# Kernel tuning notes

Measured on AMD Instinct MI355X. Metric: run time of the kernel, lower is better.

## Reference

```python
import jax, jax.numpy as jnp
import numpy as np

NUM_V, NUM_R, ARITY = 100000, 1000, 3
D, I, H = 128, 64, 128
B, N = 4096, 64


def setup_inputs() -> dict:
    key = jax.random.key(0)
    ks = jax.random.split(key, 11)
    return {
        "r": jax.random.randint(ks[0], (B, N), 0, NUM_R),
        "e": jax.random.randint(ks[1], (ARITY, B, N), 0, NUM_V),
        "V": jax.random.normal(ks[2], (NUM_V, D + I), dtype=jnp.float32),
        "R": jax.random.normal(ks[3], (NUM_R, D), dtype=jnp.float32),
        "P": jax.random.normal(ks[4], (ARITY, D), dtype=jnp.float32),
        "WV": jax.random.normal(ks[5], (D + I, H), dtype=jnp.float32) * (1.0 / np.sqrt(D + I)),
        "bV": jax.random.normal(ks[6], (H,), dtype=jnp.float32) * 0.01,
        "WR": jax.random.normal(ks[7], (D, H), dtype=jnp.float32) * (1.0 / np.sqrt(D)),
        "bR": jax.random.normal(ks[8], (H,), dtype=jnp.float32) * 0.01,
        "WP": jax.random.normal(ks[9], (D, H), dtype=jnp.float32) * (1.0 / np.sqrt(D)),
        "bP": jax.random.normal(ks[10], (H,), dtype=jnp.float32) * 0.01,
    }


def reference(r, e, V, R, P, WV, bV, WR, bR, WP, bP):
    # x = Rl(R[r]) : gather relation embeddings then project -> [B, N, H]
    x = jnp.einsum("bnd,dh->bnh", R[r], WR) + bR
    # Pl(P[i]) for all arity positions at once -> [A, H]
    pe = P @ WP + bP
    # Vl(V[e[i]]) for all positions: gather then project -> [A, B, N, H]
    ve = jnp.einsum("abnd,dh->abnh", V[e], WV) + bV
    # loop body x = x * Pl(P[i]) * Vl(V[e[i]]) == product over arity axis
    x = x * jnp.prod(pe[:, None, None, :] * ve, axis=0)
    # dropout is identity (p=0 / eval); reduce over neighbor axis
    return jnp.sum(x, axis=1)  # [B, H]
```

## Files before the change

### kernel.cpp

```cpp
#include <hip/hip_runtime.h>

#define NUM_V 100000
#define NUM_R 1000
#define ARITY 3
#define DD 128
#define DI 192
#define HH 128
#define BB 4096
#define NN 64

typedef __attribute__((ext_vector_type(4))) float f32x4;
typedef __attribute__((ext_vector_type(8))) _Float16 half8;
typedef __attribute__((ext_vector_type(2))) _Float16 half2v;

__device__ inline void gload16(const void* g, void* lds) {
    __builtin_amdgcn_global_load_lds(
        (const __attribute__((address_space(1))) unsigned int*)g,
        (__attribute__((address_space(3))) unsigned int*)lds, 16, 0, 0);
}

__global__ __launch_bounds__(256) void prep_kernel(
    const float* __restrict__ R, const float* __restrict__ WR, const float* __restrict__ bR,
    _Float16* __restrict__ RWh,
    const float* __restrict__ WV, unsigned short* __restrict__ wf,
    const float* __restrict__ P, const float* __restrict__ WP, const float* __restrict__ bP,
    float* __restrict__ peProd) {
    const int bid = blockIdx.x;
    const int tid = threadIdx.x;

    if (bid < 32) {
        const int lane = tid & 63;
        const int wave = tid >> 6;
        const int wavesPerGrid = 32 * 4;
        const int waveId = bid * 4 + wave;
        const float2 b2 = ((const float2*)bR)[lane];
        const float2* __restrict__ W2 = (const float2*)WR;
        for (int rowBase0 = waveId * 8; rowBase0 < NUM_R; rowBase0 += wavesPerGrid * 8) {
            const int rowBase = __builtin_amdgcn_readfirstlane(rowBase0);
            float2 acc[8];
#pragma unroll
            for (int r8 = 0; r8 < 8; ++r8) acc[r8] = make_float2(0.f, 0.f);
#pragma unroll 4
            for (int k4 = 0; k4 < DD / 4; ++k4) {
                float4 v[8];
#pragma unroll
                for (int r8 = 0; r8 < 8; ++r8)
                    v[r8] = ((const float4*)(R + (size_t)(rowBase + r8) * DD))[k4];
#pragma unroll
                for (int kk = 0; kk < 4; ++kk) {
                    float2 w = W2[(k4 * 4 + kk) * 64 + lane];
#pragma unroll
                    for (int r8 = 0; r8 < 8; ++r8) {
                        float vv = (kk == 0) ? v[r8].x : (kk == 1) ? v[r8].y : (kk == 2) ? v[r8].z : v[r8].w;
                        acc[r8].x += vv * w.x;
                        acc[r8].y += vv * w.y;
                    }
                }
            }
#pragma unroll
            for (int r8 = 0; r8 < 8; ++r8) {
                if (rowBase + r8 < NUM_R) {
                    half2v h;
                    h.x = (_Float16)(acc[r8].x + b2.x);
                    h.y = (_Float16)(acc[r8].y + b2.y);
                    *(half2v*)(RWh + (size_t)(rowBase + r8) * HH + lane * 2) = h;
                }
            }
        }
    } else if (bid < 80) {
        if (tid < 64) {
            const int wb = bid - 32;
            const int ks = wb >> 3;
            const int ct = wb & 7;
            const int l = tid;
            const int col = ct * 16 + (l & 15);
            const int k0 = ks * 32 + (l >> 4) * 8;
            size_t base = (size_t)(ks * 8 + ct) * 512;
#pragma unroll
            for (int j = 0; j < 8; ++j) {
                float v = WV[(size_t)(k0 + j) * HH + col];
                wf[base + l * 8 + j] = __builtin_bit_cast(unsigned short, (_Float16)v);
            }
        }
    } else {
        if (tid < HH) {
            int h = tid;
            float prod = 1.0f;
            for (int a = 0; a < ARITY; ++a) {
                float acc = bP[h];
                for (int d = 0; d < DD; ++d) acc += P[a * DD + d] * WP[d * HH + h];
                prod *= acc;
            }
            peProd[h] = prod;
        }
    }
}

__global__ __launch_bounds__(832, 6) void gemm_bres(const float* __restrict__ A,
                                                    const unsigned short* __restrict__ wf,
                                                    const float* __restrict__ bias,
                                                    _Float16* __restrict__ C, int M) {
    __shared__ unsigned short bsm[24576];

    const int tid = threadIdx.x;
    const int l = tid & 63;
    const int wv = tid >> 6;

    const int tile = wv * 512 + blockIdx.x;
    const int rowbase = tile * 16;
    const bool active = rowbase < M;

    float bcol[8];
#pragma unroll
    for (int ct = 0; ct < 8; ++ct) bcol[ct] = bias[ct * 16 + (l & 15)];

    const float* aptr;
    {
        int rr = rowbase + (l & 15);
        if (rr >= M) rr = M - 1;
        aptr = A + (size_t)rr * DI + (l >> 4) * 8;
    }

    f32x4 acc[8];
#pragma unroll
    for (int ct = 0; ct < 8; ++ct) acc[ct] = (f32x4){0.f, 0.f, 0.f, 0.f};

    float4 va[3][2];
#define LOAD_A(buf, ks)                                   \
    do {                                                  \
        va[buf][0] = *(const float4*)(aptr + (ks) * 32);  \
        va[buf][1] = *(const float4*)(aptr + (ks) * 32 + 4); \
    } while (0)

    if (active) {
        LOAD_A(0, 0);
        LOAD_A(1, 1);
    }

    if (wv < 12) {
#pragma unroll
        for (int i = 0; i < 4; ++i) {
            const int off = wv * 4096 + i * 1024;
            gload16((const char*)wf + off + l * 16, (char*)bsm + off);
        }
    }

    __syncthreads();
    if (!active) return;

#pragma unroll
    for (int ks = 0; ks < 6; ++ks) {
        const int cur = ks % 3;
        if (ks < 4) LOAD_A((ks + 2) % 3, ks + 2);

        half8 ah;
        {
            half8 t;
            t[0] = (_Float16)va[cur][0].x;
            t[1] = (_Float16)va[cur][0].y;
            t[2] = (_Float16)va[cur][0].z;
            t[3] = (_Float16)va[cur][0].w;
            t[4] = (_Float16)va[cur][1].x;
            t[5] = (_Float16)va[cur][1].y;
            t[6] = (_Float16)va[cur][1].z;
            t[7] = (_Float16)va[cur][1].w;
            ah = t;
        }

#pragma unroll
        for (int ct = 0; ct < 8; ++ct) {
            const int fb = (ks * 8 + ct) * 512;
            half8 bh = *(const half8*)&bsm[fb + l * 8];
            acc[ct] = __builtin_amdgcn_mfma_f32_16x16x32_f16(ah, bh, acc[ct], 0, 0, 0);
        }
    }
#undef LOAD_A

    {
        const int rb = rowbase + (l >> 4) * 4;
#pragma unroll
        for (int j = 0; j < 4; ++j) {
            const int row = rb + j;
            if (row < M) {
#pragma unroll
                for (int ct = 0; ct < 8; ++ct)
                    C[(size_t)row * HH + ct * 16 + (l & 15)] = (_Float16)(acc[ct][j] + bcol[ct]);
            }
        }
    }
}

__global__ __launch_bounds__(256) void gather_kernel(const int* __restrict__ r,
                                                     const int* __restrict__ e,
                                                     const _Float16* __restrict__ VWh,
                                                     const _Float16* __restrict__ RWh,
                                                     const float* __restrict__ peProd,
                                                     float* __restrict__ out) {
    __shared__ int rIdx[NN];
    __shared__ int eIdx[ARITY][NN];
    __shared__ float4 partial[3][16][2];

    const int b = blockIdx.x;
    const int tid = threadIdx.x;

    if (tid < NN) {
        rIdx[tid] = r[b * NN + tid];
    } else {
        int t = tid - NN;
        eIdx[t >> 6][t & 63] = e[(size_t)(t >> 6) * BB * NN + b * NN + (t & 63)];
    }
    __syncthreads();

    const int lane = tid & 63;
    const int wv = tid >> 6;
    const int q = lane >> 4;
    const int ho = lane & 15;

    float acc8[8];
#pragma unroll
    for (int k = 0; k < 8; ++k) acc8[k] = 0.f;

#pragma unroll
    for (int it = 0; it < 4; ++it) {
        int n = it * 16 + wv * 4 + q;
        half8 rw = *(const half8*)(RWh + (size_t)rIdx[n] * HH + ho * 8);
        half8 v0 = *(const half8*)(VWh + (size_t)eIdx[0][n] * HH + ho * 8);
        half8 v1 = *(const half8*)(VWh + (size_t)eIdx[1][n] * HH + ho * 8);
        half8 v2 = *(const half8*)(VWh + (size_t)eIdx[2][n] * HH + ho * 8);
        half8 p = rw * v0;
        p = p * v1;
        p = p * v2;
#pragma unroll
        for (int k = 0; k < 8; ++k) acc8[k] += (float)p[k];
    }

#pragma unroll
    for (int k = 0; k < 8; ++k) {
        acc8[k] += __shfl_xor(acc8[k], 16);
        acc8[k] += __shfl_xor(acc8[k], 32);
    }

    if (wv > 0 && lane < 16) {
        partial[wv - 1][ho][0] = make_float4(acc8[0], acc8[1], acc8[2], acc8[3]);
        partial[wv - 1][ho][1] = make_float4(acc8[4], acc8[5], acc8[6], acc8[7]);
    }
    __syncthreads();
    if (wv == 0 && lane < 16) {
        float4 s0 = make_float4(acc8[0], acc8[1], acc8[2], acc8[3]);
        float4 s1 = make_float4(acc8[4], acc8[5], acc8[6], acc8[7]);
#pragma unroll
        for (int g = 0; g < 3; ++g) {
            float4 t0 = partial[g][ho][0], t1 = partial[g][ho][1];
            s0.x += t0.x; s0.y += t0.y; s0.z += t0.z; s0.w += t0.w;
            s1.x += t1.x; s1.y += t1.y; s1.z += t1.z; s1.w += t1.w;
        }
        float4 p0 = ((const float4*)peProd)[ho * 2];
        float4 p1 = ((const float4*)peProd)[ho * 2 + 1];
        ((float4*)(out + (size_t)b * HH))[ho * 2] =
            make_float4(s0.x * p0.x, s0.y * p0.y, s0.z * p0.z, s0.w * p0.w);
        ((float4*)(out + (size_t)b * HH))[ho * 2 + 1] =
            make_float4(s1.x * p1.x, s1.y * p1.y, s1.z * p1.z, s1.w * p1.w);
    }
}

extern "C" void kernel_launch(void* const* d_in, const int* in_sizes, int n_in,
                              void* d_out, int out_size, void* d_ws, size_t ws_size,
                              hipStream_t stream) {
    const int* r = (const int*)d_in[0];
    const int* e = (const int*)d_in[1];
    const float* V = (const float*)d_in[2];
    const float* R = (const float*)d_in[3];
    const float* P = (const float*)d_in[4];
    const float* WV = (const float*)d_in[5];
    const float* bV = (const float*)d_in[6];
    const float* WR = (const float*)d_in[7];
    const float* bR = (const float*)d_in[8];
    const float* WP = (const float*)d_in[9];
    const float* bP = (const float*)d_in[10];
    float* out = (float*)d_out;

    _Float16* VWh = (_Float16*)d_ws;
    _Float16* RWh = VWh + (size_t)NUM_V * HH;
    float* peProd = (float*)(RWh + (size_t)NUM_R * HH);
    unsigned short* wfrag = (unsigned short*)(peProd + HH);

    prep_kernel<<<81, 256, 0, stream>>>(R, WR, bR, RWh, WV, wfrag, P, WP, bP, peProd);
    gemm_bres<<<512, 832, 0, stream>>>(V, wfrag, bV, VWh, NUM_V);
    gather_kernel<<<BB, 256, 0, stream>>>(r, e, VWh, RWh, peProd, out);
}
```

Measured before the change: 68.71 us.

## Fuse prep kernel into V-projection GEMM and convert WV fragments in-block

Removes the separate prep kernel launch. Each GEMM block now converts WV from fp32 into the fp16 fragment layout directly in LDS, replacing the async global-to-LDS copy of a precomputed fragment buffer. The R projection and the arity product are appended to the tail of the GEMM blocks, spread across 500 blocks plus one extra block. This saves a launch and a dependency, but every block now redoes the strided WV conversion, and the tail blocks run a serial scalar dot-product loop that may lengthen the critical path.

```diff
diff --git a/kernel.cpp b/kernel.cpp
--- a/kernel.cpp
+++ b/kernel.cpp
@@ -13,106 +13,26 @@
 typedef __attribute__((ext_vector_type(8))) _Float16 half8;
 typedef __attribute__((ext_vector_type(2))) _Float16 half2v;
 
-__device__ inline void gload16(const void* g, void* lds) {
-    __builtin_amdgcn_global_load_lds(
-        (const __attribute__((address_space(1))) unsigned int*)g,
-        (__attribute__((address_space(3))) unsigned int*)lds, 16, 0, 0);
-}
-
-__global__ __launch_bounds__(256) void prep_kernel(
+__global__ __launch_bounds__(832, 6) void gemm_fused(
+    const float* __restrict__ A, const float* __restrict__ WV, const float* __restrict__ bV,
     const float* __restrict__ R, const float* __restrict__ WR, const float* __restrict__ bR,
-    _Float16* __restrict__ RWh,
-    const float* __restrict__ WV, unsigned short* __restrict__ wf,
     const float* __restrict__ P, const float* __restrict__ WP, const float* __restrict__ bP,
-    float* __restrict__ peProd) {
-    const int bid = blockIdx.x;
-    const int tid = threadIdx.x;
-
-    if (bid < 32) {
-        const int lane = tid & 63;
-        const int wave = tid >> 6;
-        const int wavesPerGrid = 32 * 4;
-        const int waveId = bid * 4 + wave;
-        const float2 b2 = ((const float2*)bR)[lane];
-        const float2* __restrict__ W2 = (const float2*)WR;
-        for (int rowBase0 = waveId * 8; rowBase0 < NUM_R; rowBase0 += wavesPerGrid * 8) {
-            const int rowBase = __builtin_amdgcn_readfirstlane(rowBase0);
-            float2 acc[8];
-#pragma unroll
-            for (int r8 = 0; r8 < 8; ++r8) acc[r8] = make_float2(0.f, 0.f);
-#pragma unroll 4
-            for (int k4 = 0; k4 < DD / 4; ++k4) {
-                float4 v[8];
-#pragma unroll
-                for (int r8 = 0; r8 < 8; ++r8)
-                    v[r8] = ((const float4*)(R + (size_t)(rowBase + r8) * DD))[k4];
-#pragma unroll
-                for (int kk = 0; kk < 4; ++kk) {
-                    float2 w = W2[(k4 * 4 + kk) * 64 + lane];
-#pragma unroll
-                    for (int r8 = 0; r8 < 8; ++r8) {
-                        float vv = (kk == 0) ? v[r8].x : (kk == 1) ? v[r8].y : (kk == 2) ? v[r8].z : v[r8].w;
-                        acc[r8].x += vv * w.x;
-                        acc[r8].y += vv * w.y;
-                    }
-                }
-            }
-#pragma unroll
-            for (int r8 = 0; r8 < 8; ++r8) {
-                if (rowBase + r8 < NUM_R) {
-                    half2v h;
-                    h.x = (_Float16)(acc[r8].x + b2.x);
-                    h.y = (_Float16)(acc[r8].y + b2.y);
-                    *(half2v*)(RWh + (size_t)(rowBase + r8) * HH + lane * 2) = h;
-                }
-            }
-        }
-    } else if (bid < 80) {
-        if (tid < 64) {
-            const int wb = bid - 32;
-            const int ks = wb >> 3;
-            const int ct = wb & 7;
-            const int l = tid;
-            const int col = ct * 16 + (l & 15);
-            const int k0 = ks * 32 + (l >> 4) * 8;
-            size_t base = (size_t)(ks * 8 + ct) * 512;
-#pragma unroll
-            for (int j = 0; j < 8; ++j) {
-                float v = WV[(size_t)(k0 + j) * HH + col];
-                wf[base + l * 8 + j] = __builtin_bit_cast(unsigned short, (_Float16)v);
-            }
-        }
-    } else {
-        if (tid < HH) {
-            int h = tid;
-            float prod = 1.0f;
-            for (int a = 0; a < ARITY; ++a) {
-                float acc = bP[h];
-                for (int d = 0; d < DD; ++d) acc += P[a * DD + d] * WP[d * HH + h];
-                prod *= acc;
-            }
-            peProd[h] = prod;
-        }
-    }
-}
-
-__global__ __launch_bounds__(832, 6) void gemm_bres(const float* __restrict__ A,
-                                                    const unsigned short* __restrict__ wf,
-                                                    const float* __restrict__ bias,
-                                                    _Float16* __restrict__ C, int M) {
+    _Float16* __restrict__ VWh, _Float16* __restrict__ RWh, float* __restrict__ peProd,
+    int M) {
     __shared__ unsigned short bsm[24576];
 
     const int tid = threadIdx.x;
     const int l = tid & 63;
     const int wv = tid >> 6;
-
-    const int tile = wv * 512 + blockIdx.x;
+    const int bid = blockIdx.x;
+
+    const int tile = wv * 512 + bid;
     const int rowbase = tile * 16;
     const bool active = rowbase < M;
 
     float bcol[8];
 #pragma unroll
-    for (int ct = 0; ct < 8; ++ct) bcol[ct] = bias[ct * 16 + (l & 15)];
+    for (int ct = 0; ct < 8; ++ct) bcol[ct] = bV[ct * 16 + (l & 15)];
 
     const float* aptr;
     {
@@ -126,9 +46,9 @@
     for (int ct = 0; ct < 8; ++ct) acc[ct] = (f32x4){0.f, 0.f, 0.f, 0.f};
 
     float4 va[3][2];
-#define LOAD_A(buf, ks)                                   \
-    do {                                                  \
-        va[buf][0] = *(const float4*)(aptr + (ks) * 32);  \
+#define LOAD_A(buf, ks)                                      \
+    do {                                                     \
+        va[buf][0] = *(const float4*)(aptr + (ks) * 32);     \
         va[buf][1] = *(const float4*)(aptr + (ks) * 32 + 4); \
     } while (0)
 
@@ -137,46 +57,53 @@
         LOAD_A(1, 1);
     }
 
-    if (wv < 12) {
+    if (tid < 768) {
 #pragma unroll
         for (int i = 0; i < 4; ++i) {
-            const int off = wv * 4096 + i * 1024;
-            gload16((const char*)wf + off + l * 16, (char*)bsm + off);
+            const int g = i * 768 + tid;
+            const int ks = g >> 9;
+            const int ct = (g >> 6) & 7;
+            const int ln = g & 63;
+            const int col = ct * 16 + (ln & 15);
+            const int kbase = ks * 32 + ((ln >> 4) << 3);
+            half8 hv;
+#pragma unroll
+            for (int j = 0; j < 8; ++j)
+                hv[j] = (_Float16)WV[(size_t)(kbase + j) * HH + col];
+            *(half8*)&bsm[(size_t)g * 8] = hv;
         }
     }
 
     __syncthreads();
-    if (!active) return;
-
-#pragma unroll
-    for (int ks = 0; ks < 6; ++ks) {
-        const int cur = ks % 3;
-        if (ks < 4) LOAD_A((ks + 2) % 3, ks + 2);
-
-        half8 ah;
-        {
-            half8 t;
-            t[0] = (_Float16)va[cur][0].x;
-            t[1] = (_Float16)va[cur][0].y;
-            t[2] = (_Float16)va[cur][0].z;
-            t[3] = (_Float16)va[cur][0].w;
-            t[4] = (_Float16)va[cur][1].x;
-            t[5] = (_Float16)va[cur][1].y;
-            t[6] = (_Float16)va[cur][1].z;
-            t[7] = (_Float16)va[cur][1].w;
-            ah = t;
-        }
-
-#pragma unroll
-        for (int ct = 0; ct < 8; ++ct) {
-            const int fb = (ks * 8 + ct) * 512;
-            half8 bh = *(const half8*)&bsm[fb + l * 8];
-            acc[ct] = __builtin_amdgcn_mfma_f32_16x16x32_f16(ah, bh, acc[ct], 0, 0, 0);
-        }
-    }
-#undef LOAD_A
-
-    {
+
+    if (active) {
+#pragma unroll
+        for (int ks = 0; ks < 6; ++ks) {
+            const int cur = ks % 3;
+            if (ks < 4) LOAD_A((ks + 2) % 3, ks + 2);
+
+            half8 ah;
+            {
+                half8 t;
+                t[0] = (_Float16)va[cur][0].x;
+                t[1] = (_Float16)va[cur][0].y;
+                t[2] = (_Float16)va[cur][0].z;
+                t[3] = (_Float16)va[cur][0].w;
+                t[4] = (_Float16)va[cur][1].x;
+                t[5] = (_Float16)va[cur][1].y;
+                t[6] = (_Float16)va[cur][1].z;
+                t[7] = (_Float16)va[cur][1].w;
+                ah = t;
+            }
+
+#pragma unroll
+            for (int ct = 0; ct < 8; ++ct) {
+                const int fb = (ks * 8 + ct) * 512;
+                half8 bh = *(const half8*)&bsm[fb + l * 8];
+                acc[ct] = __builtin_amdgcn_mfma_f32_16x16x32_f16(ah, bh, acc[ct], 0, 0, 0);
+            }
+        }
+
         const int rb = rowbase + (l >> 4) * 4;
 #pragma unroll
         for (int j = 0; j < 4; ++j) {
@@ -184,8 +111,31 @@
             if (row < M) {
 #pragma unroll
                 for (int ct = 0; ct < 8; ++ct)
-                    C[(size_t)row * HH + ct * 16 + (l & 15)] = (_Float16)(acc[ct][j] + bcol[ct]);
-            }
+                    VWh[(size_t)row * HH + ct * 16 + (l & 15)] = (_Float16)(acc[ct][j] + bcol[ct]);
+            }
+        }
+    }
+#undef LOAD_A
+
+    if (bid < 500) {
+        if (tid < 256) {
+            const int row = bid * 2 + (tid >> 7);
+            const int col = tid & 127;
+            float a2 = bR[col];
+            const float* Rr = R + (size_t)row * DD;
+            for (int d = 0; d < DD; ++d) a2 += Rr[d] * WR[(size_t)d * HH + col];
+            RWh[(size_t)row * HH + col] = (_Float16)a2;
+        }
+    } else if (bid == 511) {
+        if (tid < HH) {
+            const int h = tid;
+            float prod = 1.0f;
+            for (int a = 0; a < ARITY; ++a) {
+                float a2 = bP[h];
+                for (int d = 0; d < DD; ++d) a2 += P[a * DD + d] * WP[d * HH + h];
+                prod *= a2;
+            }
+            peProd[h] = prod;
         }
     }
 }
@@ -282,9 +232,8 @@
     _Float16* VWh = (_Float16*)d_ws;
     _Float16* RWh = VWh + (size_t)NUM_V * HH;
     float* peProd = (float*)(RWh + (size_t)NUM_R * HH);
-    unsigned short* wfrag = (unsigned short*)(peProd + HH);
-
-    prep_kernel<<<81, 256, 0, stream>>>(R, WR, bR, RWh, WV, wfrag, P, WP, bP, peProd);
-    gemm_bres<<<512, 832, 0, stream>>>(V, wfrag, bV, VWh, NUM_V);
+
+    gemm_fused<<<512, 832, 0, stream>>>(V, WV, bV, R, WR, bR, P, WP, bP,
+                                        VWh, RWh, peProd, NUM_V);
     gather_kernel<<<BB, 256, 0, stream>>>(r, e, VWh, RWh, peProd, out);
 }
```

Result: faster. 60.15 us (-12.5%).
